# Kernel optimization log

Hardware: AMD Instinct MI355X
Metric: run time of the kernel (lower is better)

Reference implementation:

```python
import jax, jax.numpy as jnp
import numpy as np

B, N, D = 64, 4096, 512
ATT = 128


def setup_inputs() -> dict:
    key = jax.random.key(0)
    ks = jax.random.split(key, 7)
    s = lambda fan_in: 1.0 / np.sqrt(fan_in)
    return {
        "v_I": jax.random.normal(ks[0], (B, N, D), dtype=jnp.float32),
        "v_Q": jax.random.normal(ks[1], (B, D), dtype=jnp.float32),
        "W_I": jax.random.normal(ks[2], (D, ATT), dtype=jnp.float32) * s(D),
        "W_Q": jax.random.normal(ks[3], (D, ATT), dtype=jnp.float32) * s(D),
        "b_Q": jnp.zeros((ATT,), dtype=jnp.float32),
        "W_p": jax.random.normal(ks[4], (ATT, 1), dtype=jnp.float32) * s(ATT),
        "b_p": jnp.zeros((1,), dtype=jnp.float32),
    }


def reference(v_I, v_Q, W_I, W_Q, b_Q, W_p, b_p):
    # v_I: [B, N, D], v_Q: [B, D]
    v_I_att = jnp.tanh(jnp.einsum("bnd,da->bna", v_I, W_I))          # [B, N, A]
    v_Q_att = jnp.tanh(v_Q @ W_Q + b_Q)[:, None, :]                  # [B, 1, A]
    h_A = jnp.tanh(v_I_att + v_Q_att)                                # [B, N, A]
    # dropout is identity in inference/reference mode
    p_I = (jnp.einsum("bna,ao->bno", h_A, W_p) + b_p)[..., 0]        # [B, N]
    p_I_output = jax.nn.softmax(p_I, axis=-1)                        # [B, N]
    v_att = jnp.einsum("bn,bnd->bd", p_I_output, v_I)                # [B, D]
    u = v_att + v_Q                                                  # [B, D]
    return (p_I_output, u)
```

## Files before the change

kernel.cpp:

```cpp
#include <hip/hip_runtime.h>
#include <cstdint>
#include <cstddef>

#define B_ 64
#define N_ 4096
#define D_ 512
#define A_ 128

typedef unsigned short u16;
typedef __attribute__((ext_vector_type(8))) short bf16x8;
typedef __attribute__((ext_vector_type(4))) float f32x4;

__device__ __forceinline__ u16 cvt_bf16(float x) {
    unsigned u = __float_as_uint(x);
    return (u16)((u + 0x7FFFu + ((u >> 16) & 1u)) >> 16);
}
__device__ __forceinline__ unsigned pack2_bf16(float a, float b) {
    unsigned ua = __float_as_uint(a), ub = __float_as_uint(b);
    unsigned ra = (ua + 0x7FFFu + ((ua >> 16) & 1u)) >> 16;
    unsigned rb = (ub + 0x7FFFu + ((ub >> 16) & 1u)) >> 16;
    return ra | (rb << 16);
}
__device__ __forceinline__ float bf2f(unsigned lo16) {
    return __uint_as_float(lo16 << 16);
}
__device__ __forceinline__ float fast_tanh(float x) {
    float ax = fabsf(x);
    float e  = __expf(-2.0f * ax);
    float r  = __fdividef(1.0f - e, 1.0f + e);
    return x < 0.0f ? -r : r;
}
__device__ __forceinline__ void gl_lds16(const void* g, void* l) {
    __builtin_amdgcn_global_load_lds(
        (const __attribute__((address_space(1))) unsigned int*)g,
        (__attribute__((address_space(3))) unsigned int*)l, 16, 0, 0);
}

#define WAITVM(N) asm volatile("s_waitcnt vmcnt(" #N ")" ::: "memory")
#define SCHEDB()  __builtin_amdgcn_sched_barrier(0)

__global__ void k_prep(const float* __restrict__ WI, const float* __restrict__ vQ,
                       const float* __restrict__ WQ, const float* __restrict__ bQ,
                       u16* __restrict__ Wbf, float* __restrict__ qatt,
                       float* __restrict__ sums, float* __restrict__ u_raw) {
    const int blk = blockIdx.x, t = threadIdx.x;
    if (blk < 64) {
        #pragma unroll
        for (int i = 0; i < 2; ++i) {
            int item = blk * 256 + i * 128 + t;
            int a  = item & 127;
            int d0 = (item >> 7) << 2;
            ushort4 r;
            r.x = cvt_bf16(WI[(d0 + 0) * A_ + a]);
            r.y = cvt_bf16(WI[(d0 + 1) * A_ + a]);
            r.z = cvt_bf16(WI[(d0 + 2) * A_ + a]);
            r.w = cvt_bf16(WI[(d0 + 3) * A_ + a]);
            int off = (a >> 4) * 8192
                    + (d0 >> 5) * 512
                    + ((d0 >> 3) & 3) * 128
                    + (a & 15) * 8
                    + (d0 & 7);
            *(ushort4*)&Wbf[off] = r;
        }
    } else {
        const int b = blk - 64;
        __shared__ float sq[D_];
        for (int d = t; d < D_; d += 128) sq[d] = vQ[b * D_ + d];
        __syncthreads();
        float acc = bQ[t];
        #pragma unroll 8
        for (int d = 0; d < D_; ++d) acc += sq[d] * WQ[d * A_ + t];
        qatt[b * A_ + t] = fast_tanh(acc);
        float4 z = {0.f, 0.f, 0.f, 0.f};
        *(float4*)(u_raw + b * D_ + t * 4) = z;
        if (t == 0) sums[b] = 0.0f;
    }
}

__global__ void __launch_bounds__(512, 4)
k_fused(const float* __restrict__ vI, const u16* __restrict__ Wbf,
        const float* __restrict__ qatt, const float* __restrict__ Wp,
        float* __restrict__ wbuf, float* __restrict__ sums,
        float* __restrict__ u_raw) {
    const int b  = blockIdx.y;
    const int n0 = blockIdx.x * 64;
    const int t    = threadIdx.x;
    const int lane = t & 63, wave = t >> 6;
    const int l15  = lane & 15, quad = lane >> 4;
    const int rg = wave >> 1, cg = wave & 1;

    __shared__ __align__(16) char smem[81920];
    u16*  sA = (u16*)smem;
    char* sB = smem + 65536;
    float* sph  = (float*)sB;
    float* sw   = (float*)(sB + 8192);
    float* sred = (float*)(sB + 8448);

    float qa[4], wp[4];
    #pragma unroll
    for (int nt = 0; nt < 4; ++nt) {
        int a = (cg * 4 + nt) * 16 + l15;
        qa[nt] = qatt[b * A_ + a];
        wp[nt] = Wp[a];
    }
    SCHEDB();

    const int ar  = t >> 3;
    const int akx = t & 7;
    const float* ag = vI + ((size_t)(b * N_ + n0 + ar) * D_ + akx * 8);
    char* awb = (char*)sA + ar * 1024 + ((akx * 16) ^ ((ar & 7) << 4));

    const u16* bsrc = Wbf + (size_t)(wave * 16) * 512 + lane * 8;
    char* bdst = sB + wave * 2048;

    const int arow = rg * 16 + l15;
    const char* afb = (const char*)sA + arow * 1024;
    const int aswz = (arow & 7) << 4;
    const char* bfb = sB + (cg * 4) * 2048 + lane * 16;

    f32x4 acc[4];
    #pragma unroll
    for (int i = 0; i < 4; ++i) acc[i] = (f32x4){0.f, 0.f, 0.f, 0.f};

    float4 areg[2][2];
    areg[0][0] = *(const float4*)(ag + 0);
    areg[0][1] = *(const float4*)(ag + 4);
    WAITVM(2);
    SCHEDB();

    #pragma unroll
    for (int kr = 0; kr < 8; ++kr) {
        gl_lds16(bsrc + (kr * 2 + 0) * 512, bdst);
        gl_lds16(bsrc + (kr * 2 + 1) * 512, bdst + 1024);
        SCHEDB();
        if (kr < 7) {
            areg[(kr + 1) & 1][0] = *(const float4*)(ag + (kr + 1) * 64);
            areg[(kr + 1) & 1][1] = *(const float4*)(ag + (kr + 1) * 64 + 4);
        }
        SCHEDB();
        if (kr < 7) { WAITVM(4); } else { WAITVM(2); }
        {
            float4 x0 = areg[kr & 1][0], x1 = areg[kr & 1][1];
            union { bf16x8 v; unsigned u[4]; } cv;
            cv.u[0] = pack2_bf16(x0.x, x0.y);
            cv.u[1] = pack2_bf16(x0.z, x0.w);
            cv.u[2] = pack2_bf16(x1.x, x1.y);
            cv.u[3] = pack2_bf16(x1.z, x1.w);
            *(bf16x8*)(awb + kr * 128) = cv.v;
        }
        SCHEDB();
        if (kr < 7) { WAITVM(2); } else { WAITVM(0); }
        asm volatile("s_waitcnt lgkmcnt(0)" ::: "memory");
        __builtin_amdgcn_s_barrier();
        SCHEDB();
        __builtin_amdgcn_s_setprio(1);
        #pragma unroll
        for (int ks = 0; ks < 2; ++ks) {
            bf16x8 af = *(const bf16x8*)(afb + kr * 128 + ((ks * 64 + quad * 16) ^ aswz));
            #pragma unroll
            for (int nt = 0; nt < 4; ++nt) {
                bf16x8 bv = *(const bf16x8*)(bfb + nt * 2048 + ks * 1024);
                acc[nt] = __builtin_amdgcn_mfma_f32_16x16x32_bf16(af, bv, acc[nt], 0, 0, 0);
            }
        }
        __builtin_amdgcn_s_setprio(0);
        SCHEDB();
        __builtin_amdgcn_s_barrier();
        SCHEDB();
    }

    #pragma unroll
    for (int r = 0; r < 4; ++r) {
        float s = 0.f;
        #pragma unroll
        for (int nt = 0; nt < 4; ++nt) {
            float t1 = fast_tanh(acc[nt][r]);
            float h  = fast_tanh(t1 + qa[nt]);
            s += h * wp[nt];
        }
        s += __shfl_xor(s, 1, 16);
        s += __shfl_xor(s, 2, 16);
        s += __shfl_xor(s, 4, 16);
        s += __shfl_xor(s, 8, 16);
        if (l15 == 0) sred[cg * 64 + rg * 16 + quad * 4 + r] = s;
    }
    __syncthreads();
    if (t < 64) {
        float we = __expf(sred[t] + sred[64 + t]);
        sw[t] = we;
        wbuf[(size_t)b * N_ + n0 + t] = we;
        float ls = we;
        ls += __shfl_xor(ls, 1);
        ls += __shfl_xor(ls, 2);
        ls += __shfl_xor(ls, 4);
        ls += __shfl_xor(ls, 8);
        ls += __shfl_xor(ls, 16);
        ls += __shfl_xor(ls, 32);
        if (t == 0) atomicAdd(sums + b, ls);
    }
    __syncthreads();

    const int dg = t & 127;
    const int rr = t >> 7;
    float p0 = 0.f, p1 = 0.f, p2 = 0.f, p3 = 0.f;
    #pragma unroll
    for (int i = 0; i < 16; ++i) {
        int n = i * 4 + rr;
        const char* src = (const char*)sA + n * 1024 + ((dg * 8) ^ ((n & 7) << 4));
        uint2 wv = *(const uint2*)src;
        float wn = sw[n];
        p0 += wn * bf2f(wv.x & 0xffffu);
        p1 += wn * bf2f(wv.x >> 16);
        p2 += wn * bf2f(wv.y & 0xffffu);
        p3 += wn * bf2f(wv.y >> 16);
    }
    *(float4*)(sph + rr * 512 + dg * 4) = (float4){p0, p1, p2, p3};
    __syncthreads();
    {
        int d = t;
        float v = sph[d] + sph[512 + d] + sph[1024 + d] + sph[1536 + d];
        atomicAdd(u_raw + (size_t)b * D_ + d, v);
    }
}

__global__ void __launch_bounds__(256)
k_fin(const float* __restrict__ wbuf, const float* __restrict__ sums,
      const float* __restrict__ u_raw, const float* __restrict__ vQ,
      float* __restrict__ p_out, float* __restrict__ u_out) {
    const int b = blockIdx.x, q = blockIdx.y, t = threadIdx.x;
    const float inv = 1.0f / sums[b];
    {
        size_t off = (size_t)b * N_ + q * 1024 + t * 4;
        float4 x = *(const float4*)(wbuf + off);
        float4 y = { x.x * inv, x.y * inv, x.z * inv, x.w * inv };
        *(float4*)(p_out + off) = y;
    }
    if (q == 0 && t < 128) {
        float4 ur = *(const float4*)(u_raw + b * D_ + t * 4);
        float4 vq = *(const float4*)(vQ + b * D_ + t * 4);
        float4 o  = { ur.x * inv + vq.x, ur.y * inv + vq.y,
                      ur.z * inv + vq.z, ur.w * inv + vq.w };
        *(float4*)(u_out + b * D_ + t * 4) = o;
    }
}

extern "C" void kernel_launch(void* const* d_in, const int* in_sizes, int n_in,
                              void* d_out, int out_size, void* d_ws, size_t ws_size,
                              hipStream_t stream) {
    const float* vI = (const float*)d_in[0];
    const float* vQ = (const float*)d_in[1];
    const float* WI = (const float*)d_in[2];
    const float* WQ = (const float*)d_in[3];
    const float* bQ = (const float*)d_in[4];
    const float* Wp = (const float*)d_in[5];

    float* out_p = (float*)d_out;
    float* out_u = out_p + (size_t)B_ * N_;

    char* ws = (char*)d_ws;
    u16*   Wbf   = (u16*)ws;
    float* qatt  = (float*)(ws + 131072);
    float* sums  = (float*)(ws + 163840);
    float* u_raw = (float*)(ws + 164864);
    float* wbuf  = (float*)(ws + 295936);

    k_prep<<<128, 128, 0, stream>>>(WI, vQ, WQ, bQ, Wbf, qatt, sums, u_raw);
    k_fused<<<dim3(N_ / 64, B_), 512, 0, stream>>>(vI, Wbf, qatt, Wp,
                                                   wbuf, sums, u_raw);
    k_fin<<<dim3(B_, 4), 256, 0, stream>>>(wbuf, sums, u_raw, vQ, out_p, out_u);
}
```

Before: 748.8 us.

## Load W_I bf16 fragments directly into registers, drop LDS staging and second barrier

The B operand (bf16 W_I) no longer goes through LDS via global_load_lds. Each wave now loads its own MFMA fragments straight into a double-buffered register array (16 bf16x8), prefetching the next k-slice. Because B no longer lives in LDS, the trailing per-iteration barrier is removed, LDS shrinks, and the qatt/Wp loads move after the main loop. This adds register pressure and redundant global/L2 traffic, since each wave pair re-reads the same W fragments, but it removes LDS writes and a barrier per k-step.

```diff
diff --git a/kernel.cpp b/kernel.cpp
--- a/kernel.cpp
+++ b/kernel.cpp
@@ -29,11 +29,6 @@
     float e  = __expf(-2.0f * ax);
     float r  = __fdividef(1.0f - e, 1.0f + e);
     return x < 0.0f ? -r : r;
-}
-__device__ __forceinline__ void gl_lds16(const void* g, void* l) {
-    __builtin_amdgcn_global_load_lds(
-        (const __attribute__((address_space(1))) unsigned int*)g,
-        (__attribute__((address_space(3))) unsigned int*)l, 16, 0, 0);
 }
 
 #define WAITVM(N) asm volatile("s_waitcnt vmcnt(" #N ")" ::: "memory")
@@ -89,58 +84,52 @@
     const int l15  = lane & 15, quad = lane >> 4;
     const int rg = wave >> 1, cg = wave & 1;
 
-    __shared__ __align__(16) char smem[81920];
-    u16*  sA = (u16*)smem;
-    char* sB = smem + 65536;
-    float* sph  = (float*)sB;
-    float* sw   = (float*)(sB + 8192);
-    float* sred = (float*)(sB + 8448);
-
-    float qa[4], wp[4];
-    #pragma unroll
-    for (int nt = 0; nt < 4; ++nt) {
-        int a = (cg * 4 + nt) * 16 + l15;
-        qa[nt] = qatt[b * A_ + a];
-        wp[nt] = Wp[a];
-    }
-    SCHEDB();
+    __shared__ __align__(16) char smem[74496];
+    u16*   sA   = (u16*)smem;
+    float* sph  = (float*)(smem + 65536);
+    float* sw   = (float*)(smem + 73728);
+    float* sred = (float*)(smem + 73984);
 
     const int ar  = t >> 3;
     const int akx = t & 7;
     const float* ag = vI + ((size_t)(b * N_ + n0 + ar) * D_ + akx * 8);
     char* awb = (char*)sA + ar * 1024 + ((akx * 16) ^ ((ar & 7) << 4));
 
-    const u16* bsrc = Wbf + (size_t)(wave * 16) * 512 + lane * 8;
-    char* bdst = sB + wave * 2048;
+    const u16* bg = Wbf + lane * 8;
 
     const int arow = rg * 16 + l15;
     const char* afb = (const char*)sA + arow * 1024;
     const int aswz = (arow & 7) << 4;
-    const char* bfb = sB + (cg * 4) * 2048 + lane * 16;
 
     f32x4 acc[4];
     #pragma unroll
     for (int i = 0; i < 4; ++i) acc[i] = (f32x4){0.f, 0.f, 0.f, 0.f};
 
-    float4 areg[2][2];
+    float4  areg[2][2];
+    bf16x8  breg[2][8];
+
     areg[0][0] = *(const float4*)(ag + 0);
     areg[0][1] = *(const float4*)(ag + 4);
-    WAITVM(2);
     SCHEDB();
+    #pragma unroll
+    for (int nt = 0; nt < 4; ++nt) {
+        breg[0][nt * 2 + 0] = *(const bf16x8*)(bg + ((((cg * 4 + nt) * 16) + 0) << 9));
+        breg[0][nt * 2 + 1] = *(const bf16x8*)(bg + ((((cg * 4 + nt) * 16) + 1) << 9));
+    }
+    SCHEDB();
 
     #pragma unroll
     for (int kr = 0; kr < 8; ++kr) {
-        gl_lds16(bsrc + (kr * 2 + 0) * 512, bdst);
-        gl_lds16(bsrc + (kr * 2 + 1) * 512, bdst + 1024);
+        const int cur = kr & 1, nxt = cur ^ 1;
+        WAITVM(8);
         SCHEDB();
         if (kr < 7) {
-            areg[(kr + 1) & 1][0] = *(const float4*)(ag + (kr + 1) * 64);
-            areg[(kr + 1) & 1][1] = *(const float4*)(ag + (kr + 1) * 64 + 4);
-        }
-        SCHEDB();
-        if (kr < 7) { WAITVM(4); } else { WAITVM(2); }
+            areg[nxt][0] = *(const float4*)(ag + (kr + 1) * 64);
+            areg[nxt][1] = *(const float4*)(ag + (kr + 1) * 64 + 4);
+        }
+        SCHEDB();
         {
-            float4 x0 = areg[kr & 1][0], x1 = areg[kr & 1][1];
+            float4 x0 = areg[cur][0], x1 = areg[cur][1];
             union { bf16x8 v; unsigned u[4]; } cv;
             cv.u[0] = pack2_bf16(x0.x, x0.y);
             cv.u[1] = pack2_bf16(x0.z, x0.w);
@@ -149,8 +138,17 @@
             *(bf16x8*)(awb + kr * 128) = cv.v;
         }
         SCHEDB();
-        if (kr < 7) { WAITVM(2); } else { WAITVM(0); }
+        if (kr < 7) {
+            #pragma unroll
+            for (int nt = 0; nt < 4; ++nt) {
+                breg[nxt][nt * 2 + 0] = *(const bf16x8*)(bg + ((((cg * 4 + nt) * 16) + (kr + 1) * 2 + 0) << 9));
+                breg[nxt][nt * 2 + 1] = *(const bf16x8*)(bg + ((((cg * 4 + nt) * 16) + (kr + 1) * 2 + 1) << 9));
+            }
+        }
+        SCHEDB();
+        if (kr < 7) { WAITVM(10); } else { WAITVM(0); }
         asm volatile("s_waitcnt lgkmcnt(0)" ::: "memory");
+        SCHEDB();
         __builtin_amdgcn_s_barrier();
         SCHEDB();
         __builtin_amdgcn_s_setprio(1);
@@ -158,17 +156,20 @@
         for (int ks = 0; ks < 2; ++ks) {
             bf16x8 af = *(const bf16x8*)(afb + kr * 128 + ((ks * 64 + quad * 16) ^ aswz));
             #pragma unroll
-            for (int nt = 0; nt < 4; ++nt) {
-                bf16x8 bv = *(const bf16x8*)(bfb + nt * 2048 + ks * 1024);
-                acc[nt] = __builtin_amdgcn_mfma_f32_16x16x32_bf16(af, bv, acc[nt], 0, 0, 0);
-            }
+            for (int nt = 0; nt < 4; ++nt)
+                acc[nt] = __builtin_amdgcn_mfma_f32_16x16x32_bf16(af, breg[cur][nt * 2 + ks], acc[nt], 0, 0, 0);
         }
         __builtin_amdgcn_s_setprio(0);
         SCHEDB();
-        __builtin_amdgcn_s_barrier();
-        SCHEDB();
-    }
-
+    }
+
+    float qa[4], wp[4];
+    #pragma unroll
+    for (int nt = 0; nt < 4; ++nt) {
+        int a = (cg * 4 + nt) * 16 + l15;
+        qa[nt] = qatt[b * A_ + a];
+        wp[nt] = Wp[a];
+    }
     #pragma unroll
     for (int r = 0; r < 4; ++r) {
         float s = 0.f;
```

Result: no change. 748.0 us (-0.1%).
